# Kernel optimization log

Measured on AMD Instinct MI355X. Metric: run time of the kernel, lower is better.

## Reference

```python
import jax, jax.numpy as jnp
import numpy as np

V, E, S_MAX, H, L = 32000, 1024, 2048, 16, 6
D = E // H  # head_dim = 64
EPS = 1e-5


def _ln(x, g, b):
    mu = jnp.mean(x, axis=-1, keepdims=True)
    var = jnp.mean(jnp.square(x - mu), axis=-1, keepdims=True)
    return (x - mu) * jax.lax.rsqrt(var + EPS) * g + b


def setup_inputs() -> dict:
    key = jax.random.key(0)
    ks = iter(jax.random.split(key, 32))
    std = 0.02
    B, S = 1, 2048
    inp = {
        "tokens": jax.random.randint(next(ks), (B, S), 0, V, dtype=jnp.int32),
        "W_emb": jax.random.normal(next(ks), (V, E), jnp.float32) * std,  # tied with fc_out
        "W_pos": jax.random.normal(next(ks), (S_MAX, E), jnp.float32) * std,
        # per-layer stacked params [L, ...]
        "Wq": jax.random.normal(next(ks), (L, E, E), jnp.float32) * std,
        "Wk": jax.random.normal(next(ks), (L, E, E), jnp.float32) * std,
        "Wv": jax.random.normal(next(ks), (L, E, E), jnp.float32) * std,
        "Wo": jax.random.normal(next(ks), (L, E, E), jnp.float32) * std,
        "bo": jnp.zeros((L, E), jnp.float32),
        "ln1_g": jnp.ones((L, E), jnp.float32),
        "ln1_b": jnp.zeros((L, E), jnp.float32),
        "ln2_g": jnp.ones((L, E), jnp.float32),
        "ln2_b": jnp.zeros((L, E), jnp.float32),
        "W1": jax.random.normal(next(ks), (L, 4 * E, E), jnp.float32) * std,
        "b1": jnp.zeros((L, 4 * E), jnp.float32),
        "W2": jax.random.normal(next(ks), (L, E, 4 * E), jnp.float32) * std,
        "b2": jnp.zeros((L, E), jnp.float32),
        "lnf_g": jnp.ones((E,), jnp.float32),
        "lnf_b": jnp.zeros((E,), jnp.float32),
    }
    return inp


def _gpt_forward(tokens, W_emb, W_pos, Wq, Wk, Wv, Wo, bo, ln1_g, ln1_b,
                 ln2_g, ln2_b, W1, b1, W2, b2, lnf_g, lnf_b):
    B, S = tokens.shape
    x = W_emb[tokens] + W_pos[:S][None, :, :]  # [B,S,E]
    causal = jnp.tril(jnp.ones((S, S), bool))  # [S,S]
    scale = 1.0 / np.sqrt(D)

    def block(x, p):
        wq, wk, wv, wo, bo_, g1, b1n, g2, b2n, w1, bf1, w2, bf2 = p
        h = _ln(x, g1, b1n)
        # torch Linear: y = x @ W.T ; split heads -> [B,H,S,D]
        def heads(w):
            return (h @ w.T).reshape(B, S, H, D).transpose(0, 2, 1, 3)
        q, k, v = heads(wq), heads(wk), heads(wv)
        scores = jnp.einsum('bhqd,bhkd->bhqk', q, k) * scale
        scores = jnp.where(causal[None, None], scores, -jnp.inf)
        attn = jax.nn.softmax(scores, axis=-1)
        o = jnp.einsum('bhqk,bhkd->bhqd', attn, v)
        o = o.transpose(0, 2, 1, 3).reshape(B, S, E)
        x = x + o @ wo.T + bo_
        h2 = _ln(x, g2, b2n)
        ff = jax.nn.gelu(h2 @ w1.T + bf1, approximate=False) @ w2.T + bf2
        return x + ff, None

    params = (Wq, Wk, Wv, Wo, bo, ln1_g, ln1_b, ln2_g, ln2_b, W1, b1, W2, b2)
    x, _ = jax.lax.scan(block, x, params)
    x = _ln(x, lnf_g, lnf_b)
    return x @ W_emb.T  # tied output projection [B,S,V]


def reference(tokens, W_emb, W_pos, Wq, Wk, Wv, Wo, bo, ln1_g, ln1_b,
              ln2_g, ln2_b, W1, b1, W2, b2, lnf_g, lnf_b):
    return _gpt_forward(tokens, W_emb, W_pos, Wq, Wk, Wv, Wo, bo, ln1_g,
                        ln1_b, ln2_g, ln2_b, W1, b1, W2, b2, lnf_g, lnf_b)
```

## Files before the change

### kernel.cpp

```cpp
#include <hip/hip_runtime.h>
#include <math.h>

#define S_LEN 2048
#define EMB 1024
#define NHEAD 16
#define HDIM 64
#define NLAYER 6
#define VOCAB 32000
#define FFDIM 4096

using f32x4 = __attribute__((ext_vector_type(4))) float;
using bf16x8 = __attribute__((ext_vector_type(8))) __bf16;
typedef unsigned short us;

static __device__ __forceinline__ unsigned short f2bf(float f) {
  union { float f; unsigned int u; } v; v.f = f;
  unsigned int r = v.u + 0x7FFFu + ((v.u >> 16) & 1u);
  return (unsigned short)(r >> 16);
}

#define GLOAD_LDS16(g, l)                                                      \
  __builtin_amdgcn_global_load_lds(                                            \
      (const __attribute__((address_space(1))) void*)(g),                      \
      (__attribute__((address_space(3))) void*)(l), 16, 0, 0)

__global__ __launch_bounds__(256) void cvt_bf16_kernel(
    const float* __restrict__ in, us* __restrict__ out, long n) {
  long i = ((long)blockIdx.x * 256 + threadIdx.x) * 8;
  if (i >= n) return;
  const float4* p = (const float4*)(in + i);
  float4 a = p[0], b = p[1];
  uint4 o;
  o.x = (unsigned)f2bf(a.x) | ((unsigned)f2bf(a.y) << 16);
  o.y = (unsigned)f2bf(a.z) | ((unsigned)f2bf(a.w) << 16);
  o.z = (unsigned)f2bf(b.x) | ((unsigned)f2bf(b.y) << 16);
  o.w = (unsigned)f2bf(b.z) | ((unsigned)f2bf(b.w) << 16);
  *(uint4*)(out + i) = o;
}

__global__ __launch_bounds__(256) void embed_kernel(
    const int* __restrict__ tok, const float* __restrict__ Wemb,
    const float* __restrict__ Wpos, float* __restrict__ x) {
  int s = blockIdx.x, t = threadIdx.x;
  int tk = tok[s];
  const float4* we = (const float4*)(Wemb + (size_t)tk * EMB);
  const float4* wp = (const float4*)(Wpos + (size_t)s * EMB);
  float4 a = we[t], b = wp[t];
  float4 o; o.x = a.x + b.x; o.y = a.y + b.y; o.z = a.z + b.z; o.w = a.w + b.w;
  ((float4*)(x + (size_t)s * EMB))[t] = o;
}

__global__ __launch_bounds__(256) void ln_kernel(
    const float* __restrict__ x, const float* __restrict__ g,
    const float* __restrict__ b, us* __restrict__ out) {
  int row = blockIdx.x, t = threadIdx.x, lane = t & 63, wave = t >> 6;
  float4 v = ((const float4*)(x + (size_t)row * EMB))[t];
  float s = v.x + v.y + v.z + v.w;
  float q = v.x * v.x + v.y * v.y + v.z * v.z + v.w * v.w;
  #pragma unroll
  for (int d = 1; d < 64; d <<= 1) { s += __shfl_xor(s, d); q += __shfl_xor(q, d); }
  __shared__ float rs[4], rq[4];
  if (lane == 0) { rs[wave] = s; rq[wave] = q; }
  __syncthreads();
  s = rs[0] + rs[1] + rs[2] + rs[3];
  q = rq[0] + rq[1] + rq[2] + rq[3];
  float mean = s * (1.0f / EMB);
  float var = q * (1.0f / EMB) - mean * mean;
  float rstd = rsqrtf(var + 1e-5f);
  float4 gg = ((const float4*)g)[t], bb = ((const float4*)b)[t];
  ushort4 o;
  o.x = f2bf((v.x - mean) * rstd * gg.x + bb.x);
  o.y = f2bf((v.y - mean) * rstd * gg.y + bb.y);
  o.z = f2bf((v.z - mean) * rstd * gg.z + bb.z);
  o.w = f2bf((v.w - mean) * rstd * gg.w + bb.w);
  ((ushort4*)(out + (size_t)row * EMB))[t] = o;
}

template <int SK>
__global__ __launch_bounds__(256) void reduce_ln_kernel(
    float* __restrict__ x, const float* __restrict__ p,
    const float* __restrict__ bias, const float* __restrict__ g,
    const float* __restrict__ b, us* __restrict__ out) {
  int row = blockIdx.x, t = threadIdx.x, lane = t & 63, wave = t >> 6;
  const size_t plane = (size_t)S_LEN * EMB;
  float4 v = ((const float4*)(x + (size_t)row * EMB))[t];
  float4 bb4 = ((const float4*)bias)[t];
  v.x += bb4.x; v.y += bb4.y; v.z += bb4.z; v.w += bb4.w;
  #pragma unroll
  for (int z = 0; z < SK; ++z) {
    float4 q4 = ((const float4*)(p + z * plane + (size_t)row * EMB))[t];
    v.x += q4.x; v.y += q4.y; v.z += q4.z; v.w += q4.w;
  }
  ((float4*)(x + (size_t)row * EMB))[t] = v;
  float s = v.x + v.y + v.z + v.w;
  float q = v.x * v.x + v.y * v.y + v.z * v.z + v.w * v.w;
  #pragma unroll
  for (int d = 1; d < 64; d <<= 1) { s += __shfl_xor(s, d); q += __shfl_xor(q, d); }
  __shared__ float rs[4], rq[4];
  if (lane == 0) { rs[wave] = s; rq[wave] = q; }
  __syncthreads();
  s = rs[0] + rs[1] + rs[2] + rs[3];
  q = rq[0] + rq[1] + rq[2] + rq[3];
  float mean = s * (1.0f / EMB);
  float var = q * (1.0f / EMB) - mean * mean;
  float rstd = rsqrtf(var + 1e-5f);
  float4 gg = ((const float4*)g)[t], lb = ((const float4*)b)[t];
  ushort4 o;
  o.x = f2bf((v.x - mean) * rstd * gg.x + lb.x);
  o.y = f2bf((v.y - mean) * rstd * gg.y + lb.y);
  o.z = f2bf((v.z - mean) * rstd * gg.z + lb.z);
  o.w = f2bf((v.w - mean) * rstd * gg.w + lb.w);
  ((ushort4*)(out + (size_t)row * EMB))[t] = o;
}

template <int HAS_BIAS, int HAS_RES, int DO_GELU, int OUT_BF16>
__global__ __launch_bounds__(256) void gemm_bb(
    const us* __restrict__ A, const us* __restrict__ B0,
    const us* __restrict__ B1, const us* __restrict__ B2,
    const float* __restrict__ bias, const float* __restrict__ res,
    void* C0, void* C1, void* C2, int M, int N, int K) {
  const us* B = blockIdx.z == 0 ? B0 : (blockIdx.z == 1 ? B1 : B2);
  void* C = blockIdx.z == 0 ? C0 : (blockIdx.z == 1 ? C1 : C2);
  const int nwg = gridDim.x * gridDim.y;
  int lin = blockIdx.y * gridDim.x + blockIdx.x;
  {
    const int qx = nwg >> 3, r = nwg & 7;
    const int xcd = lin & 7, idx = lin >> 3;
    lin = (xcd < r ? xcd * (qx + 1) : r * (qx + 1) + (xcd - r) * qx) + idx;
  }
  const int m0 = (lin % gridDim.x) * 128, n0 = (lin / gridDim.x) * 128;
  const int t = threadIdx.x, lane = t & 63, wave = t >> 6;
  const int wm = (wave >> 1) * 64, wn = (wave & 1) * 64;
  __shared__ __align__(16) us As[128 * 64];
  __shared__ __align__(16) us Bs[128 * 64];
  f32x4 acc[4][4] = {};
  const int kIters = K >> 6;
  const int cbase = wave * 64;
  const int myc = cbase + lane;
  for (int kt = 0; kt < kIters; ++kt) {
    const int k0 = kt << 6;
    __syncthreads();
    #pragma unroll
    for (int i = 0; i < 4; ++i) {
      const int c = myc + i * 256;
      const int row = c >> 3, col = (c & 7) * 8;
      GLOAD_LDS16(A + (size_t)(m0 + row) * K + k0 + col,
                  As + (size_t)(cbase + i * 256) * 8);
    }
    #pragma unroll
    for (int i = 0; i < 4; ++i) {
      const int c = myc + i * 256;
      const int row = c >> 3, col = (c & 7) * 8;
      GLOAD_LDS16(B + (size_t)(n0 + row) * K + k0 + col,
                  Bs + (size_t)(cbase + i * 256) * 8);
    }
    __syncthreads();
    #pragma unroll
    for (int ks = 0; ks < 2; ++ks) {
      bf16x8 af[4], bfr[4];
      #pragma unroll
      for (int i = 0; i < 4; ++i)
        af[i] = *(const bf16x8*)(As + (wm + i * 16 + (lane & 15)) * 64 + ks * 32 + (lane >> 4) * 8);
      #pragma unroll
      for (int j = 0; j < 4; ++j)
        bfr[j] = *(const bf16x8*)(Bs + (wn + j * 16 + (lane & 15)) * 64 + ks * 32 + (lane >> 4) * 8);
      #pragma unroll
      for (int i = 0; i < 4; ++i)
        #pragma unroll
        for (int j = 0; j < 4; ++j)
          acc[i][j] = __builtin_amdgcn_mfma_f32_16x16x32_bf16(af[i], bfr[j], acc[i][j], 0, 0, 0);
    }
  }
  const int r0 = (lane >> 4) * 4, cl = lane & 15;
  #pragma unroll
  for (int i = 0; i < 4; ++i) {
    #pragma unroll
    for (int j = 0; j < 4; ++j) {
      const int col = n0 + wn + j * 16 + cl;
      float bv = HAS_BIAS ? bias[col] : 0.0f;
      #pragma unroll
      for (int r = 0; r < 4; ++r) {
        const int row = m0 + wm + i * 16 + r0 + r;
        float val = acc[i][j][r] + bv;
        if (DO_GELU) val = val * 0.5f * (1.0f + erff(val * 0.70710678118f));
        if (HAS_RES) val += res[(size_t)row * N + col];
        if (OUT_BF16) ((us*)C)[(size_t)row * N + col] = f2bf(val);
        else          ((float*)C)[(size_t)row * N + col] = val;
      }
    }
  }
}

__global__ __launch_bounds__(256) void gemm_sk(
    const us* __restrict__ A, const us* __restrict__ B,
    float* __restrict__ C, int M, int N, int K, int kSlice) {
  const int z = blockIdx.z;
  const int nwg = gridDim.x * gridDim.y;
  int lin = blockIdx.y * gridDim.x + blockIdx.x;
  {
    const int qx = nwg >> 3, r = nwg & 7;
    const int xcd = lin & 7, idx = lin >> 3;
    lin = (xcd < r ? xcd * (qx + 1) : r * (qx + 1) + (xcd - r) * qx) + idx;
  }
  const int m0 = (lin % gridDim.x) * 128, n0 = (lin / gridDim.x) * 128;
  const int t = threadIdx.x, lane = t & 63, wave = t >> 6;
  const int wm = (wave >> 1) * 64, wn = (wave & 1) * 64;
  __shared__ __align__(16) us As[128 * 64];
  __shared__ __align__(16) us Bs[128 * 64];
  f32x4 acc[4][4] = {};
  const int cbase = wave * 64;
  const int myc = cbase + lane;
  const int kBeg = z * kSlice;
  const int kIters = kSlice >> 6;
  for (int kt = 0; kt < kIters; ++kt) {
    const int k0 = kBeg + (kt << 6);
    __syncthreads();
    #pragma unroll
    for (int i = 0; i < 4; ++i) {
      const int c = myc + i * 256;
      const int row = c >> 3, col = (c & 7) * 8;
      GLOAD_LDS16(A + (size_t)(m0 + row) * K + k0 + col,
                  As + (size_t)(cbase + i * 256) * 8);
    }
    #pragma unroll
    for (int i = 0; i < 4; ++i) {
      const int c = myc + i * 256;
      const int row = c >> 3, col = (c & 7) * 8;
      GLOAD_LDS16(B + (size_t)(n0 + row) * K + k0 + col,
                  Bs + (size_t)(cbase + i * 256) * 8);
    }
    __syncthreads();
    #pragma unroll
    for (int ks = 0; ks < 2; ++ks) {
      bf16x8 af[4], bfr[4];
      #pragma unroll
      for (int i = 0; i < 4; ++i)
        af[i] = *(const bf16x8*)(As + (wm + i * 16 + (lane & 15)) * 64 + ks * 32 + (lane >> 4) * 8);
      #pragma unroll
      for (int j = 0; j < 4; ++j)
        bfr[j] = *(const bf16x8*)(Bs + (wn + j * 16 + (lane & 15)) * 64 + ks * 32 + (lane >> 4) * 8);
      #pragma unroll
      for (int i = 0; i < 4; ++i)
        #pragma unroll
        for (int j = 0; j < 4; ++j)
          acc[i][j] = __builtin_amdgcn_mfma_f32_16x16x32_bf16(af[i], bfr[j], acc[i][j], 0, 0, 0);
    }
  }
  float* Cz = C + (size_t)z * M * N;
  const int r0 = (lane >> 4) * 4, cl = lane & 15;
  #pragma unroll
  for (int i = 0; i < 4; ++i)
    #pragma unroll
    for (int j = 0; j < 4; ++j) {
      const int col = n0 + wn + j * 16 + cl;
      #pragma unroll
      for (int r = 0; r < 4; ++r)
        Cz[(size_t)(m0 + wm + i * 16 + r0 + r) * N + col] = acc[i][j][r];
    }
}

__global__ __launch_bounds__(512, 2) void gemm_v256(
    const us* __restrict__ A, const us* __restrict__ B,
    float* __restrict__ C, int M, int N, int K) {
  const int nwg = gridDim.x * gridDim.y;
  int lin = blockIdx.y * gridDim.x + blockIdx.x;
  {
    const int qx = nwg >> 3, r = nwg & 7;
    const int xcd = lin & 7, idx = lin >> 3;
    lin = (xcd < r ? xcd * (qx + 1) : r * (qx + 1) + (xcd - r) * qx) + idx;
  }
  const int m0 = (lin % gridDim.x) * 256, n0 = (lin / gridDim.x) * 256;
  const int t = threadIdx.x, lane = t & 63, wave = t >> 6;
  const int lq = lane & 15, hi = lane >> 4;
  const int wm = (wave >> 2) * 128, wn = (wave & 3) * 64;
  __shared__ __align__(16) us As[2][256 * 64];
  __shared__ __align__(16) us Bs[2][256 * 64];
  f32x4 acc[8][4] = {};
  const int kIters = K >> 6;
  const int ldsbase = (wave * 64) * 8;

  {
    const int k0 = 0;
    #pragma unroll
    for (int i = 0; i < 4; ++i) {
      const int c = t + i * 512;
      const int row = c >> 3, col = (c & 7) * 8;
      GLOAD_LDS16(A + (size_t)(m0 + row) * K + k0 + col, &As[0][0] + ldsbase + i * 512 * 8);
      GLOAD_LDS16(B + (size_t)(n0 + row) * K + k0 + col, &Bs[0][0] + ldsbase + i * 512 * 8);
    }
  }
  __syncthreads();
  int cur = 0;
  for (int kt = 0; kt < kIters; ++kt) {
    if (kt + 1 < kIters) {
      const int k0 = (kt + 1) << 6;
      #pragma unroll
      for (int i = 0; i < 4; ++i) {
        const int c = t + i * 512;
        const int row = c >> 3, col = (c & 7) * 8;
        GLOAD_LDS16(A + (size_t)(m0 + row) * K + k0 + col,
                    &As[cur ^ 1][0] + ldsbase + i * 512 * 8);
        GLOAD_LDS16(B + (size_t)(n0 + row) * K + k0 + col,
                    &Bs[cur ^ 1][0] + ldsbase + i * 512 * 8);
      }
    }
    #pragma unroll
    for (int ks = 0; ks < 2; ++ks) {
      bf16x8 bfr[4];
      #pragma unroll
      for (int j = 0; j < 4; ++j)
        bfr[j] = *(const bf16x8*)(&Bs[cur][0] + (wn + j * 16 + lq) * 64 + ks * 32 + hi * 8);
      #pragma unroll
      for (int i = 0; i < 8; ++i) {
        bf16x8 af = *(const bf16x8*)(&As[cur][0] + (wm + i * 16 + lq) * 64 + ks * 32 + hi * 8);
        #pragma unroll
        for (int j = 0; j < 4; ++j)
          acc[i][j] = __builtin_amdgcn_mfma_f32_16x16x32_bf16(af, bfr[j], acc[i][j], 0, 0, 0);
      }
    }
    __syncthreads();
    cur ^= 1;
  }
  #pragma unroll
  for (int i = 0; i < 8; ++i)
    #pragma unroll
    for (int j = 0; j < 4; ++j) {
      const int col = n0 + wn + j * 16 + lq;
      #pragma unroll
      for (int r = 0; r < 4; ++r)
        C[(size_t)(m0 + wm + i * 16 + hi * 4 + r) * N + col] = acc[i][j][r];
    }
}

__global__ __launch_bounds__(256) void attn_kernel(
    const us* __restrict__ qb, const us* __restrict__ kb,
    const us* __restrict__ vb, us* __restrict__ ob) {
  const int qt = gridDim.x - 1 - blockIdx.x;
  const int head = blockIdx.y;
  const int t = threadIdx.x, lane = t & 63, wave = t >> 6;
  const int hi = lane >> 4, lq = lane & 15;
  const int hd = head * HDIM;
  const int q0w = qt * 64 + wave * 16;
  __shared__ __align__(16) us Kl[2][64 * 64];
  __shared__ __align__(16) us Vl[2][64 * 72];
  __shared__ __align__(16) us Pl[4][16][72];
  bf16x8 qf[2];
  {
    const us* qp = qb + (size_t)(q0w + lq) * EMB + hd + hi * 8;
    qf[0] = *(const bf16x8*)qp;
    qf[1] = *(const bf16x8*)(qp + 32);
    #pragma unroll
    for (int e = 0; e < 8; ++e) {
      qf[0][e] = (__bf16)((float)qf[0][e] * 0.125f);
      qf[1][e] = (__bf16)((float)qf[1][e] * 0.125f);
    }
  }
  f32x4 accO[4] = {};
  float m_run = -1e30f, l_run = 0.f;
  const int vr2 = (t >> 3) * 2, d8 = (t & 7) * 8;
  const int q_g = q0w + lq;

  {
    #pragma unroll
    for (int i = 0; i < 2; ++i) {
      const int c = wave * 64 + lane + i * 256;
      const int row = c >> 3, j = c & 7;
      const int colE = (j * 8) ^ ((row & 7) << 3);
      GLOAD_LDS16(kb + (size_t)(row) * EMB + hd + colE,
                  &Kl[0][0] + (wave * 64 + i * 256) * 8);
    }
    const us* vp = vb + (size_t)vr2 * EMB + hd + d8;
    uint4 vA = *(const uint4*)vp;
    uint4 vB = *(const uint4*)(vp + EMB);
    const unsigned* wa = (const unsigned*)&vA;
    const unsigned* wb = (const unsigned*)&vB;
    #pragma unroll
    for (int i = 0; i < 8; ++i) {
      unsigned lo = (i & 1) ? (wa[i >> 1] >> 16) : (wa[i >> 1] & 0xffffu);
      unsigned hw = (i & 1) ? (wb[i >> 1] >> 16) : (wb[i >> 1] & 0xffffu);
      *(unsigned*)(&Vl[0][0] + (d8 + i) * 72 + vr2) = lo | (hw << 16);
    }
  }
  __syncthreads();
  int cur = 0;
  for (int kt = 0; kt <= qt; ++kt) {
    uint4 vA, vB;
    if (kt < qt) {
      #pragma unroll
      for (int i = 0; i < 2; ++i) {
        const int c = wave * 64 + lane + i * 256;
        const int row = c >> 3, j = c & 7;
        const int colE = (j * 8) ^ ((row & 7) << 3);
        GLOAD_LDS16(kb + (size_t)((kt + 1) * 64 + row) * EMB + hd + colE,
                    &Kl[cur ^ 1][0] + (wave * 64 + i * 256) * 8);
      }
      const us* vp = vb + (size_t)((kt + 1) * 64 + vr2) * EMB + hd + d8;
      vA = *(const uint4*)vp;
      vB = *(const uint4*)(vp + EMB);
    }
    f32x4 sc[4] = {};
    #pragma unroll
    for (int ks = 0; ks < 2; ++ks) {
      #pragma unroll
      for (int fn = 0; fn < 4; ++fn) {
        const int rowk = fn * 16 + lq;
        const us* kp = &Kl[cur][0] + rowk * 64 + ((ks * 32 + hi * 8) ^ ((rowk & 7) << 3));
        sc[fn] = __builtin_amdgcn_mfma_f32_16x16x32_bf16(
            *(const bf16x8*)kp, qf[ks], sc[fn], 0, 0, 0);
      }
    }
    float pv[16];
    float pmax = -1e30f;
    if (kt == qt) {
      #pragma unroll
      for (int fn = 0; fn < 4; ++fn)
        #pragma unroll
        for (int r = 0; r < 4; ++r) {
          const int k_g = kt * 64 + fn * 16 + hi * 4 + r;
          float sv = sc[fn][r];
          if (k_g > q_g) sv = -1e30f;
          pv[fn * 4 + r] = sv;
          pmax = fmaxf(pmax, sv);
        }
    } else {
      #pragma unroll
      for (int fn = 0; fn < 4; ++fn)
        #pragma unroll
        for (int r = 0; r < 4; ++r) {
          float sv = sc[fn][r];
          pv[fn * 4 + r] = sv;
          pmax = fmaxf(pmax, sv);
        }
    }
    pmax = fmaxf(pmax, __shfl_xor(pmax, 16));
    pmax = fmaxf(pmax, __shfl_xor(pmax, 32));
    if (!__all(pmax <= m_run + 8.0f)) {
      const float mn = fmaxf(m_run, pmax);
      const float alpha = __expf(m_run - mn);
      m_run = mn;
      l_run *= alpha;
      float ar[4];
      #pragma unroll
      for (int r = 0; r < 4; ++r) ar[r] = __shfl(alpha, hi * 4 + r);
      #pragma unroll
      for (int df = 0; df < 4; ++df)
        #pragma unroll
        for (int r = 0; r < 4; ++r) accO[df][r] *= ar[r];
    }
    float rsum = 0.f;
    #pragma unroll
    for (int i = 0; i < 16; ++i) {
      float e = __expf(pv[i] - m_run);
      pv[i] = e;
      rsum += e;
    }
    rsum += __shfl_xor(rsum, 16);
    rsum += __shfl_xor(rsum, 32);
    l_run += rsum;
    #pragma unroll
    for (int fn = 0; fn < 4; ++fn) {
      ushort4 pk;
      pk.x = f2bf(pv[fn * 4 + 0]);
      pk.y = f2bf(pv[fn * 4 + 1]);
      pk.z = f2bf(pv[fn * 4 + 2]);
      pk.w = f2bf(pv[fn * 4 + 3]);
      *(ushort4*)&Pl[wave][lq][fn * 16 + hi * 4] = pk;
    }
    #pragma unroll
    for (int ks = 0; ks < 2; ++ks) {
      bf16x8 pf = *(const bf16x8*)&Pl[wave][lq][ks * 32 + hi * 8];
      #pragma unroll
      for (int df = 0; df < 4; ++df) {
        bf16x8 vf = *(const bf16x8*)(&Vl[cur][0] + (df * 16 + lq) * 72 + ks * 32 + hi * 8);
        accO[df] = __builtin_amdgcn_mfma_f32_16x16x32_bf16(pf, vf, accO[df], 0, 0, 0);
      }
    }
    if (kt < qt) {
      const unsigned* wa = (const unsigned*)&vA;
      const unsigned* wb = (const unsigned*)&vB;
      #pragma unroll
      for (int i = 0; i < 8; ++i) {
        unsigned lo = (i & 1) ? (wa[i >> 1] >> 16) : (wa[i >> 1] & 0xffffu);
        unsigned hw = (i & 1) ? (wb[i >> 1] >> 16) : (wb[i >> 1] & 0xffffu);
        *(unsigned*)(&Vl[cur ^ 1][0] + (d8 + i) * 72 + vr2) = lo | (hw << 16);
      }
    }
    __syncthreads();
    cur ^= 1;
  }
  float linv[4];
  #pragma unroll
  for (int r = 0; r < 4; ++r) linv[r] = 1.0f / __shfl(l_run, hi * 4 + r);
  #pragma unroll
  for (int r = 0; r < 4; ++r) {
    const int row = q0w + hi * 4 + r;
    #pragma unroll
    for (int df = 0; df < 4; ++df)
      ob[(size_t)row * EMB + hd + df * 16 + lq] = f2bf(accO[df][r] * linv[r]);
  }
}

extern "C" void kernel_launch(void* const* d_in, const int* in_sizes, int n_in,
                              void* d_out, int out_size, void* d_ws, size_t ws_size,
                              hipStream_t stream) {
  const int* tok = (const int*)d_in[0];
  const float* Wemb = (const float*)d_in[1];
  const float* Wpos = (const float*)d_in[2];
  const float* Wq = (const float*)d_in[3];
  const float* Wk = (const float*)d_in[4];
  const float* Wv = (const float*)d_in[5];
  const float* Wo = (const float*)d_in[6];
  const float* bo = (const float*)d_in[7];
  const float* ln1g = (const float*)d_in[8];
  const float* ln1b = (const float*)d_in[9];
  const float* ln2g = (const float*)d_in[10];
  const float* ln2b = (const float*)d_in[11];
  const float* W1 = (const float*)d_in[12];
  const float* b1 = (const float*)d_in[13];
  const float* W2 = (const float*)d_in[14];
  const float* b2 = (const float*)d_in[15];
  const float* lnfg = (const float*)d_in[16];
  const float* lnfb = (const float*)d_in[17];
  (void)in_sizes; (void)n_in; (void)out_size;

  const size_t MB = 1u << 20;
  char* ws = (char*)d_ws;
  float* x = (float*)ws;
  us* h  = (us*)(ws + 8 * MB);
  us* qb = (us*)(ws + 12 * MB);
  us* kb = (us*)(ws + 16 * MB);
  us* vb = (us*)(ws + 20 * MB);
  us* ob = (us*)(ws + 24 * MB);
  us* fb = (us*)(ws + 12 * MB);
  us* cWq = (us*)(ws + 28 * MB);
  us* cWk = (us*)(ws + 40 * MB);
  us* cWv = (us*)(ws + 52 * MB);
  us* cWo = (us*)(ws + 64 * MB);
  us* cW1 = (us*)(ws + 76 * MB);
  us* cW2 = (us*)(ws + 124 * MB);
  us* cWemb = (us*)(ws + 172 * MB);
  float* pbuf = (float*)(ws + 236 * MB);
  const size_t need_bf16 = 172 * MB + (size_t)VOCAB * EMB * 2;
  const bool bf16w = ws_size >= need_bf16;
  int skWo = 0, skF2 = 0;
  if (ws_size >= 236 * MB + 32 * MB)      { skWo = 2; skF2 = 4; }
  else if (ws_size >= 236 * MB + 16 * MB) { skWo = 2; skF2 = 2; }
  const bool fused = (skWo == 2 && skF2 == 4);

  embed_kernel<<<dim3(S_LEN), 256, 0, stream>>>(tok, Wemb, Wpos, x);
  if (!bf16w) return;

  const long nE2 = (long)NLAYER * EMB * EMB;
  const long nF  = (long)NLAYER * FFDIM * EMB;
  const long nV  = (long)VOCAB * EMB;
  cvt_bf16_kernel<<<(int)(nE2 / 2048), 256, 0, stream>>>(Wq, cWq, nE2);
  cvt_bf16_kernel<<<(int)(nE2 / 2048), 256, 0, stream>>>(Wk, cWk, nE2);
  cvt_bf16_kernel<<<(int)(nE2 / 2048), 256, 0, stream>>>(Wv, cWv, nE2);
  cvt_bf16_kernel<<<(int)(nE2 / 2048), 256, 0, stream>>>(Wo, cWo, nE2);
  cvt_bf16_kernel<<<(int)(nF / 2048), 256, 0, stream>>>(W1, cW1, nF);
  cvt_bf16_kernel<<<(int)(nF / 2048), 256, 0, stream>>>(W2, cW2, nF);
  cvt_bf16_kernel<<<(int)(nV / 2048), 256, 0, stream>>>(Wemb, cWemb, nV);

  ln_kernel<<<S_LEN, 256, 0, stream>>>(x, ln1g, ln1b, h);
  for (int l = 0; l < NLAYER; ++l) {
    const size_t wofs = (size_t)l * EMB * EMB;
    const size_t fofs = (size_t)l * FFDIM * EMB;
    gemm_bb<0, 0, 0, 1><<<dim3(16, 8, 3), 256, 0, stream>>>(
        h, cWq + wofs, cWk + wofs, cWv + wofs, nullptr, nullptr,
        qb, kb, vb, S_LEN, EMB, EMB);
    attn_kernel<<<dim3(32, NHEAD), 256, 0, stream>>>(qb, kb, vb, ob);
    if (fused) {
      gemm_sk<<<dim3(16, 8, 2), 256, 0, stream>>>(
          ob, cWo + wofs, pbuf, S_LEN, EMB, EMB, EMB / 2);
      reduce_ln_kernel<2><<<S_LEN, 256, 0, stream>>>(
          x, pbuf, bo + l * EMB, ln2g + l * EMB, ln2b + l * EMB, h);
      gemm_bb<1, 0, 1, 1><<<dim3(16, 32, 1), 256, 0, stream>>>(
          h, cW1 + fofs, nullptr, nullptr, b1 + l * FFDIM, nullptr,
          fb, nullptr, nullptr, S_LEN, FFDIM, EMB);
      gemm_sk<<<dim3(16, 8, 4), 256, 0, stream>>>(
          fb, cW2 + fofs, pbuf, S_LEN, EMB, FFDIM, FFDIM / 4);
      if (l < NLAYER - 1)
        reduce_ln_kernel<4><<<S_LEN, 256, 0, stream>>>(
            x, pbuf, b2 + l * EMB, ln1g + (l + 1) * EMB, ln1b + (l + 1) * EMB, h);
      else
        reduce_ln_kernel<4><<<S_LEN, 256, 0, stream>>>(
            x, pbuf, b2 + l * EMB, lnfg, lnfb, h);
    } else {
      gemm_bb<1, 1, 0, 0><<<dim3(16, 8, 1), 256, 0, stream>>>(
          ob, cWo + wofs, nullptr, nullptr, bo + l * EMB, x,
          x, nullptr, nullptr, S_LEN, EMB, EMB);
      ln_kernel<<<S_LEN, 256, 0, stream>>>(x, ln2g + l * EMB, ln2b + l * EMB, h);
      gemm_bb<1, 0, 1, 1><<<dim3(16, 32, 1), 256, 0, stream>>>(
          h, cW1 + fofs, nullptr, nullptr, b1 + l * FFDIM, nullptr,
          fb, nullptr, nullptr, S_LEN, FFDIM, EMB);
      gemm_bb<1, 1, 0, 0><<<dim3(16, 8, 1), 256, 0, stream>>>(
          fb, cW2 + fofs, nullptr, nullptr, b2 + l * EMB, x,
          x, nullptr, nullptr, S_LEN, EMB, FFDIM);
      if (l < NLAYER - 1)
        ln_kernel<<<S_LEN, 256, 0, stream>>>(x, ln1g + (l + 1) * EMB, ln1b + (l + 1) * EMB, h);
      else
        ln_kernel<<<S_LEN, 256, 0, stream>>>(x, lnfg, lnfb, h);
    }
  }
  gemm_v256<<<dim3(8, 125), 512, 0, stream>>>(
      h, cWemb, (float*)d_out, S_LEN, VOCAB, EMB);
}
```

Baseline: 1.499 ms.

## Rewrite vocab GEMM with triple-buffered K=32 stages, swizzled LDS, and phased MFMA

Replaces the double-buffered BK=64 vocab-projection GEMM with a three-stage pipeline of BK=32 tiles. The LDS layout is XOR-swizzled to reduce bank conflicts. Each iteration is split into two half-MFMA phases with explicit barriers, vmcnt waits, setprio and sched_barrier, so global-to-LDS loads overlap compute. Launch bounds drop to one block per SM, trading occupancy for the explicit schedule, and correctness now depends on hand-tuned waitcnt counts.

```diff
diff --git a/kernel.cpp b/kernel.cpp
--- a/kernel.cpp
+++ b/kernel.cpp
@@ -259,7 +259,7 @@
     }
 }
 
-__global__ __launch_bounds__(512, 2) void gemm_v256(
+__global__ __launch_bounds__(512, 1) void gemm_v8p(
     const us* __restrict__ A, const us* __restrict__ B,
     float* __restrict__ C, int M, int N, int K) {
   const int nwg = gridDim.x * gridDim.y;
@@ -272,63 +272,93 @@
   const int m0 = (lin % gridDim.x) * 256, n0 = (lin / gridDim.x) * 256;
   const int t = threadIdx.x, lane = t & 63, wave = t >> 6;
   const int lq = lane & 15, hi = lane >> 4;
-  const int wm = (wave >> 2) * 128, wn = (wave & 3) * 64;
-  __shared__ __align__(16) us As[2][256 * 64];
-  __shared__ __align__(16) us Bs[2][256 * 64];
+  const int rbase = (wave >> 2) * 128, cbase = (wave & 3) * 64;
+  __shared__ __align__(16) us As[3][256 * 32];
+  __shared__ __align__(16) us Bs[3][256 * 32];
   f32x4 acc[8][4] = {};
-  const int kIters = K >> 6;
-  const int ldsbase = (wave * 64) * 8;
-
-  {
-    const int k0 = 0;
-    #pragma unroll
-    for (int i = 0; i < 4; ++i) {
-      const int c = t + i * 512;
-      const int row = c >> 3, col = (c & 7) * 8;
-      GLOAD_LDS16(A + (size_t)(m0 + row) * K + k0 + col, &As[0][0] + ldsbase + i * 512 * 8);
-      GLOAD_LDS16(B + (size_t)(n0 + row) * K + k0 + col, &Bs[0][0] + ldsbase + i * 512 * 8);
-    }
-  }
-  __syncthreads();
-  int cur = 0;
-  for (int kt = 0; kt < kIters; ++kt) {
-    if (kt + 1 < kIters) {
-      const int k0 = (kt + 1) << 6;
-      #pragma unroll
-      for (int i = 0; i < 4; ++i) {
-        const int c = t + i * 512;
-        const int row = c >> 3, col = (c & 7) * 8;
-        GLOAD_LDS16(A + (size_t)(m0 + row) * K + k0 + col,
-                    &As[cur ^ 1][0] + ldsbase + i * 512 * 8);
-        GLOAD_LDS16(B + (size_t)(n0 + row) * K + k0 + col,
-                    &Bs[cur ^ 1][0] + ldsbase + i * 512 * 8);
-      }
-    }
-    #pragma unroll
-    for (int ks = 0; ks < 2; ++ks) {
-      bf16x8 bfr[4];
+  const int nt = K >> 5;
+
+#define STAGE_T(MAT, LDSB, TT)                                                 \
+  {                                                                            \
+    const int kk0 = (TT) << 5;                                                 \
+    _Pragma("unroll")                                                          \
+    for (int i_ = 0; i_ < 2; ++i_) {                                           \
+      const int ci = t + i_ * 512;                                             \
+      const int rr = ci >> 2, cc = ci & 3;                                     \
+      const int src = (cc ^ ((rr >> 1) & 3)) * 8;                              \
+      GLOAD_LDS16(MAT + (size_t)(((MAT == A) ? m0 : n0) + rr) * K + kk0 + src, \
+                  &LDSB[0] + (wave * 64 + i_ * 512) * 8);                      \
+    }                                                                          \
+  }
+
+  STAGE_T(A, As[0], 0); STAGE_T(B, Bs[0], 0);
+  STAGE_T(A, As[1], 1); STAGE_T(B, Bs[1], 1);
+  STAGE_T(A, As[2], 2); STAGE_T(B, Bs[2], 2);
+  asm volatile("s_waitcnt vmcnt(8)" ::: "memory");
+  __builtin_amdgcn_s_barrier();
+
+  int bb = 0;
+  for (int tt = 0; tt < nt; ++tt) {
+    const int sb = (bb + 2 >= 3) ? bb - 1 : bb + 2;
+    const us* Ab = &As[bb][0];
+    const us* Bb = &Bs[bb][0];
+    bf16x8 a0[4], b0[4];
+    #pragma unroll
+    for (int f = 0; f < 4; ++f) {
+      const int row = rbase + f * 16 + lq;
+      a0[f] = *(const bf16x8*)(Ab + row * 32 + ((hi ^ ((row >> 1) & 3)) * 8));
+    }
+    #pragma unroll
+    for (int f = 0; f < 4; ++f) {
+      const int row = cbase + f * 16 + lq;
+      b0[f] = *(const bf16x8*)(Bb + row * 32 + ((hi ^ ((row >> 1) & 3)) * 8));
+    }
+    if (tt + 2 < nt) STAGE_T(A, As[sb], tt + 2);
+    __builtin_amdgcn_s_barrier();
+    asm volatile("s_waitcnt lgkmcnt(0)" ::: "memory");
+    __builtin_amdgcn_sched_barrier(0);
+    __builtin_amdgcn_s_setprio(1);
+    #pragma unroll
+    for (int i = 0; i < 4; ++i)
       #pragma unroll
       for (int j = 0; j < 4; ++j)
-        bfr[j] = *(const bf16x8*)(&Bs[cur][0] + (wn + j * 16 + lq) * 64 + ks * 32 + hi * 8);
-      #pragma unroll
-      for (int i = 0; i < 8; ++i) {
-        bf16x8 af = *(const bf16x8*)(&As[cur][0] + (wm + i * 16 + lq) * 64 + ks * 32 + hi * 8);
-        #pragma unroll
-        for (int j = 0; j < 4; ++j)
-          acc[i][j] = __builtin_amdgcn_mfma_f32_16x16x32_bf16(af, bfr[j], acc[i][j], 0, 0, 0);
-      }
-    }
-    __syncthreads();
-    cur ^= 1;
-  }
+        acc[i][j] = __builtin_amdgcn_mfma_f32_16x16x32_bf16(a0[i], b0[j], acc[i][j], 0, 0, 0);
+    __builtin_amdgcn_s_setprio(0);
+    __builtin_amdgcn_s_barrier();
+    bf16x8 a1[4];
+    #pragma unroll
+    for (int f = 0; f < 4; ++f) {
+      const int row = rbase + 64 + f * 16 + lq;
+      a1[f] = *(const bf16x8*)(Ab + row * 32 + ((hi ^ ((row >> 1) & 3)) * 8));
+    }
+    if (tt + 2 < nt) {
+      STAGE_T(B, Bs[sb], tt + 2);
+      asm volatile("s_waitcnt vmcnt(4)" ::: "memory");
+    } else {
+      asm volatile("s_waitcnt vmcnt(0)" ::: "memory");
+    }
+    __builtin_amdgcn_s_barrier();
+    asm volatile("s_waitcnt lgkmcnt(0)" ::: "memory");
+    __builtin_amdgcn_sched_barrier(0);
+    __builtin_amdgcn_s_setprio(1);
+    #pragma unroll
+    for (int i = 0; i < 4; ++i)
+      #pragma unroll
+      for (int j = 0; j < 4; ++j)
+        acc[4 + i][j] = __builtin_amdgcn_mfma_f32_16x16x32_bf16(a1[i], b0[j], acc[4 + i][j], 0, 0, 0);
+    __builtin_amdgcn_s_setprio(0);
+    __builtin_amdgcn_s_barrier();
+    bb = (bb + 1 == 3) ? 0 : bb + 1;
+  }
+#undef STAGE_T
   #pragma unroll
   for (int i = 0; i < 8; ++i)
     #pragma unroll
     for (int j = 0; j < 4; ++j) {
-      const int col = n0 + wn + j * 16 + lq;
+      const int col = n0 + cbase + j * 16 + lq;
       #pragma unroll
       for (int r = 0; r < 4; ++r)
-        C[(size_t)(m0 + wm + i * 16 + hi * 4 + r) * N + col] = acc[i][j][r];
+        C[(size_t)(m0 + rbase + i * 16 + hi * 4 + r) * N + col] = acc[i][j][r];
     }
 }
 
@@ -602,6 +632,6 @@
         ln_kernel<<<S_LEN, 256, 0, stream>>>(x, lnfg, lnfb, h);
     }
   }
-  gemm_v256<<<dim3(8, 125), 512, 0, stream>>>(
+  gemm_v8p<<<dim3(8, 125), 512, 0, stream>>>(
       h, cWemb, (float*)d_out, S_LEN, VOCAB, EMB);
 }
```

After: 1.473 ms. Within noise of the previous version (-1.8%).
